# Performance work log

Hardware: AMD Instinct MI355X
Metric: run time of the kernel (lower is better)

The kernel has to match this reference:

```python
import jax, jax.numpy as jnp
import numpy as np

HIDDEN = 2048
GAMMA = 0.96875
SCALE_BASE = 512  # XPOS default from torchscale / Jamie-Stirling/RetNet


def _xpos(x, downscale=False):
    # x: [B, L, d]. Faithful port of XPOS with offset=0.
    B, L, d = x.shape
    half = d // 2
    # per-dim scale vector: (arange(0,d,2) + 0.4d) / (1.4d)
    scale_vec = (jnp.arange(0, d, 2, dtype=jnp.float32) + 0.4 * d) / (1.4 * d)  # [half]
    power = jnp.arange(L, dtype=jnp.float32) / SCALE_BASE                        # [L]
    scale = scale_vec[None, :] ** power[:, None]                                 # [L, half]
    # fixed_pos_embedding over `half` frequency dims
    inv_freq = 1.0 / (10000.0 ** (jnp.arange(half, dtype=jnp.float32) / half))   # [half]
    sinusoid = jnp.arange(L, dtype=jnp.float32)[:, None] * inv_freq[None, :]     # [L, half]
    sin, cos = jnp.sin(sinusoid), jnp.cos(sinusoid)
    if downscale:
        scale = 1.0 / scale
    # duplicate_interleave: [L, half] -> [L, d] with each column repeated twice
    sin_s = jnp.repeat(sin * scale, 2, axis=-1)  # [L, d]
    cos_s = jnp.repeat(cos * scale, 2, axis=-1)  # [L, d]
    # rotate_every_two
    x1 = x[..., 0::2]
    x2 = x[..., 1::2]
    rot = jnp.stack((-x2, x1), axis=-1).reshape(x.shape)
    return x * cos_s[None] + rot * sin_s[None]


def _decay_matrix(L):
    n = jnp.arange(L)[:, None]
    m = jnp.arange(L)[None, :]
    mask = n >= m
    # clamp exponent to avoid overflow where masked (torch sets NaN->0)
    D = jnp.where(mask, GAMMA ** jnp.maximum(n - m, 0).astype(jnp.float32), 0.0)
    return D  # [L, L]


def setup_inputs() -> dict:
    key = jax.random.key(0)
    kx, kq, kk, kv = jax.random.split(key, 4)
    B, S, H = 4, 2048, HIDDEN
    X = jax.random.normal(kx, (B, S, H), dtype=jnp.float32)
    W_Q = jax.random.normal(kq, (H, H), dtype=jnp.float32) / H
    W_K = jax.random.normal(kk, (H, H), dtype=jnp.float32) / H
    W_V = jax.random.normal(kv, (H, H), dtype=jnp.float32) / H
    return {"X": X, "W_Q": W_Q, "W_K": W_K, "W_V": W_V}


def reference(X, W_Q, W_K, W_V):
    B, S, H = X.shape
    Q = _xpos(X @ W_Q)                   # [B, S, H]
    K = _xpos(X @ W_K, downscale=True)   # [B, S, H]
    V = X @ W_V                          # [B, S, H]
    D = _decay_matrix(S)                 # [S, S]
    att = jnp.einsum("bnh,bmh->bnm", Q, K) * D[None]  # [B, S, S]
    return att @ V                       # [B, S, H]
```

## Files before the change

kernel.cpp:

```cpp
#include <hip/hip_runtime.h>
#include <math.h>


typedef __attribute__((ext_vector_type(8))) short short8;
typedef __attribute__((ext_vector_type(4))) float f32x4;
typedef __attribute__((ext_vector_type(4))) unsigned short us4;

#define BM 128
#define ABAND 384

static __device__ __forceinline__ unsigned short f2bf(float f) {
    unsigned int u = __float_as_uint(f);
    u += 0x7FFFu + ((u >> 16) & 1u);
    return (unsigned short)(u >> 16);
}

static __device__ __forceinline__ void gload16(const unsigned short* g, unsigned short* l) {
    __builtin_amdgcn_global_load_lds(
        (const __attribute__((address_space(1))) unsigned int*)g,
        (__attribute__((address_space(3))) unsigned int*)l, 16, 0, 0);
}

template <int STAGE, int BNt, int BKt>
__global__ __launch_bounds__(256)
void gemm_bt(const unsigned short* __restrict__ A,
             const unsigned short* __restrict__ Bt,
             void* __restrict__ Cv,
             unsigned short* __restrict__ Cq,
             unsigned short* __restrict__ Ck,
             unsigned short* __restrict__ Cvt,
             int lda, int ldb, int Kd,
             long long sA, long long sB, long long sC)
{
    constexpr int S = 2048, H = 2048;
    constexpr int NJ = BNt / 32;
    constexpr int KS = BKt / 32;
    constexpr int CR = BKt / 8;
    constexpr int RG = 64 / CR;
    constexpr int GA = 32 / RG;
    constexpr int GB = (BNt / 4) / RG;

    int bx, by, zb;
    if (STAGE == 3) {
        int id = blockIdx.x;
        int swz = (id & 7) * 45 + (id >> 3);
        zb = swz / 90;
        int t = swz - zb * 90;
        if (t < 6) {
            by = (t < 2) ? 0 : 1;
            bx = t - ((by == 0) ? 0 : 2);
        } else {
            by = 2 + (t - 6) / 6;
            bx = ((2 * by - 4) > 0 ? (2 * by - 4) : 0) + (t - 6) % 6;
        }
    } else if (STAGE == 4) {
        int id = blockIdx.x;
        int swz = (id & 7) * 128 + (id >> 3);
        bx = swz >> 6;
        int r = swz & 63;
        zb = r >> 4;
        by = 15 - (r & 15);
    } else {
        bx = blockIdx.x; by = blockIdx.y; zb = 0;
    }
    const int rowBase = by * BM;
    const int colBase = bx * BNt;

    A  += (long long)zb * sA;
    Bt += (long long)zb * sB;

    __shared__ unsigned short As[BM * BKt];
    __shared__ unsigned short Bs[BNt * BKt];

    const int tid  = threadIdx.x;
    const int wave = tid >> 6;
    const int lane = tid & 63;
    const int wm = (wave & 1) * 64;
    const int wn = (wave >> 1) * (BNt / 2);

    f32x4 acc[4][NJ];
#pragma unroll
    for (int i = 0; i < 4; ++i)
#pragma unroll
        for (int j = 0; j < NJ; ++j) acc[i][j] = (f32x4){0.f, 0.f, 0.f, 0.f};

    int kmax = Kd;
    if (STAGE == 4) { int km = rowBase + BM; kmax = km < Kd ? km : Kd; }
    int k0s = 0;
    if (STAGE == 4) {
        int kb0 = 2 * by - 4; k0s = (kb0 > 0 ? kb0 : 0) * 64;
        A -= k0s;
    }

    const int cpos = lane % CR;
    const int rig  = lane / CR;
    const int waveArow = wave * 32;
    const int waveBrow = wave * (BNt / 4);
    unsigned short* lA = As + wave * (32 * BKt);
    unsigned short* lB = Bs + wave * ((BNt / 4) * BKt);

    auto stage_tile = [&](int kb) {
#pragma unroll
        for (int g = 0; g < GA; ++g) {
            int r = waveArow + g * RG + rig;
            gload16(A + (size_t)(rowBase + r) * lda + kb + ((cpos ^ (r & 7)) * 8),
                    lA + g * 512);
        }
#pragma unroll
        for (int g = 0; g < GB; ++g) {
            int r = waveBrow + g * RG + rig;
            gload16(Bt + (size_t)(colBase + r) * ldb + kb + ((cpos ^ (r & 7)) * 8),
                    lB + g * 512);
        }
    };

    stage_tile(k0s);

    const int fr = lane & 15;
    const int qd = lane >> 4;
    const int fsw = fr & 7;

    for (int k0 = k0s; k0 < kmax; k0 += BKt) {
        __syncthreads();
        short8 aF[KS][4], bF[KS][NJ];
#pragma unroll
        for (int kk = 0; kk < KS; ++kk) {
#pragma unroll
            for (int i = 0; i < 4; ++i)
                aF[kk][i] = *(const short8*)&As[(wm + i * 16 + fr) * BKt + (((kk * 4 + qd) ^ fsw) * 8)];
#pragma unroll
            for (int j = 0; j < NJ; ++j)
                bF[kk][j] = *(const short8*)&Bs[(wn + j * 16 + fr) * BKt + (((kk * 4 + qd) ^ fsw) * 8)];
        }
        __syncthreads();
        if (k0 + BKt < kmax) stage_tile(k0 + BKt);
#pragma unroll
        for (int kk = 0; kk < KS; ++kk)
#pragma unroll
            for (int i = 0; i < 4; ++i)
#pragma unroll
                for (int j = 0; j < NJ; ++j)
                    acc[i][j] = __builtin_amdgcn_mfma_f32_16x16x32_bf16(aF[kk][i], bF[kk][j], acc[i][j], 0, 0, 0);
    }

    if (STAGE == 1) {
        const int mode = colBase >> 11;
        if (mode < 2) {
            unsigned short* Co = (mode == 0) ? Cq : Ck;
            const float psgn = (mode == 1) ? -1.953125e-3f : 1.953125e-3f;
#pragma unroll
            for (int j = 0; j < NJ; ++j) {
                int gc = (colBase & 2047) + wn + j * 16 + fr;
                float c0 = (float)(gc & ~1);
                float l2sv = log2f((c0 + 819.2f) * (1.0f / 2867.2f)) * psgn;
                float invf = exp2f(c0 * -0.0064881407f);
                float s1, c1;
                sincosf(invf, &s1, &c1);
#pragma unroll
                for (int i = 0; i < 4; ++i) {
                    int gr0 = rowBase + wm + i * 16 + qd * 4;
                    float fn = (float)(gr0 & (S - 1));
                    float sN, cN;
                    sincosf(fn * invf, &sN, &cN);
#pragma unroll
                    for (int r = 0; r < 4; ++r) {
                        float scale = exp2f(fn * l2sv);
                        float cs = cN * scale, ss = sN * scale;
                        float v = acc[i][j][r];
                        float o = __shfl_xor(v, 1);
                        float res = (gc & 1) ? fmaf(v, cs, o * ss) : fmaf(v, cs, -o * ss);
                        Co[(size_t)(gr0 + r) * H + gc] = f2bf(res);
                        float sn2 = sN * c1 + cN * s1;
                        cN = cN * c1 - sN * s1;
                        sN = sn2;
                        fn += 1.0f;
                    }
                }
            }
        } else {
#pragma unroll
            for (int j = 0; j < NJ; ++j) {
                int gh = (colBase & 2047) + wn + j * 16 + fr;
#pragma unroll
                for (int i = 0; i < 4; ++i) {
                    int gm0 = rowBase + wm + i * 16 + qd * 4;
                    us4 p;
#pragma unroll
                    for (int r = 0; r < 4; ++r) p[r] = f2bf(acc[i][j][r]);
                    *(us4*)&Cvt[(size_t)gh * 8192 + gm0] = p;
                }
            }
        }
    } else if (STAGE == 3) {
        unsigned short* att = (unsigned short*)Cv + (long long)zb * sC;
        const int kb0 = (2 * by - 4) > 0 ? (2 * by - 4) : 0;
        const int mshift = kb0 * 64;
#pragma unroll
        for (int j = 0; j < NJ; ++j) {
            int m = colBase + wn + j * 16 + fr;
#pragma unroll
            for (int i = 0; i < 4; ++i) {
                int n0 = rowBase + wm + i * 16 + qd * 4;
#pragma unroll
                for (int r = 0; r < 4; ++r) {
                    int d = n0 + r - m;
                    float v = (d >= 0) ? acc[i][j][r] * exp2f((float)d * -0.045803598f) : 0.0f;
                    att[(size_t)(n0 + r) * ABAND + (m - mshift)] = f2bf(v);
                }
            }
        }
    } else {
        float* Co = (float*)Cv + (long long)zb * sC;
#pragma unroll
        for (int j = 0; j < NJ; ++j) {
            int gh = colBase + wn + j * 16 + fr;
#pragma unroll
            for (int i = 0; i < 4; ++i) {
                int gn0 = rowBase + wm + i * 16 + qd * 4;
#pragma unroll
                for (int r = 0; r < 4; ++r)
                    Co[(size_t)(gn0 + r) * H + gh] = acc[i][j][r];
            }
        }
    }
}

__global__ __launch_bounds__(256)
void cvt_fused(const float* __restrict__ X, unsigned short* __restrict__ Xb,
               const float* __restrict__ W0, const float* __restrict__ W1,
               const float* __restrict__ W2, unsigned short* __restrict__ Wt) {
    __shared__ float t[64][65];
    if (blockIdx.x < 3072) {
        int id = blockIdx.x;
        int z = id >> 10, rem = id & 1023;
        const float* W = (z == 0) ? W0 : (z == 1) ? W1 : W2;
        unsigned short* Wo = Wt + (size_t)z * 4194304;
        int bx = (rem & 31) * 64, by = (rem >> 5) * 64;
        int tx = threadIdx.x & 63, ty = threadIdx.x >> 6;
#pragma unroll
        for (int r = 0; r < 64; r += 4)
            t[ty + r][tx] = W[(size_t)(by + ty + r) * 2048 + bx + tx];
        __syncthreads();
#pragma unroll
        for (int r = 0; r < 64; r += 4)
            Wo[(size_t)(bx + ty + r) * 2048 + by + tx] = f2bf(t[tx][ty + r]);
    } else {
        int id = blockIdx.x - 3072;
        const float4* X4 = (const float4*)X;
        short8* O8 = (short8*)Xb;
#pragma unroll
        for (int c = 0; c < 4; ++c) {
            size_t u = (size_t)c * (2048 * 256) + (size_t)id * 256 + threadIdx.x;
            float4 a = X4[u * 2];
            float4 b = X4[u * 2 + 1];
            short8 o;
            o[0] = f2bf(a.x); o[1] = f2bf(a.y); o[2] = f2bf(a.z); o[3] = f2bf(a.w);
            o[4] = f2bf(b.x); o[5] = f2bf(b.y); o[6] = f2bf(b.z); o[7] = f2bf(b.w);
            O8[u] = o;
        }
    }
}

extern "C" void kernel_launch(void* const* d_in, const int* in_sizes, int n_in,
                              void* d_out, int out_size, void* d_ws, size_t ws_size,
                              hipStream_t stream) {
    const int S = 2048, H = 2048;
    const long long MH = 16777216;
    const long long HH = 4194304;
    const long long SH = (long long)S * H;
    const long long SB = (long long)S * ABAND;

    const float* X  = (const float*)d_in[0];
    const float* WQ = (const float*)d_in[1];
    const float* WK = (const float*)d_in[2];
    const float* WV = (const float*)d_in[3];
    float* out = (float*)d_out;

    unsigned short* Xb    = (unsigned short*)d_ws;
    unsigned short* WtAll = Xb + MH;
    unsigned short* Qb    = WtAll + 3 * HH;
    unsigned short* Kb    = Qb + MH;
    unsigned short* Vt    = Kb + MH;
    unsigned short* att   = Vt + MH;

    cvt_fused<<<5120, 256, 0, stream>>>(X, Xb, WQ, WK, WV, WtAll);

    gemm_bt<1, 128, 64><<<dim3(48, 64), 256, 0, stream>>>(Xb, WtAll, nullptr, Qb, Kb, Vt,
                                                          H, H, H, 0, 0, 0);
    gemm_bt<3, 64, 128><<<dim3(360, 1, 1), 256, 0, stream>>>(Qb, Kb, att, nullptr, nullptr, nullptr,
                                                             H, H, H, SH, SH, SB);
    gemm_bt<4, 128, 64><<<dim3(1024, 1, 1), 256, 0, stream>>>(att, Vt, out, nullptr, nullptr, nullptr,
                                                              ABAND, 8192, S, SB, 2048, SH);
}
```

Before: 415.1 us.

## Fuse V projection with banded QK^T scores into one heterogeneous launch

Splits the QKV projection so the first launch computes only Q and K (32 column tiles). The V projection tiles then run in the same grid as the banded QK^T score tiles: 360 blocks do attention scores and 1024 blocks do V columns. The goal is to fill the GPU better, since the 360-block score launch alone underuses the CUs, and to hide its tail behind V work. The score GEMM's K-tile also drops from 128 to 64 so both roles can share one shared-memory buffer.

After: 422.0 us (median of 3 runs). Within noise of the previous version (+1.7%).

```diff
diff --git a/kernel.cpp b/kernel.cpp
--- a/kernel.cpp
+++ b/kernel.cpp
@@ -22,15 +22,17 @@
 }
 
 template <int STAGE, int BNt, int BKt>
-__global__ __launch_bounds__(256)
-void gemm_bt(const unsigned short* __restrict__ A,
-             const unsigned short* __restrict__ Bt,
-             void* __restrict__ Cv,
-             unsigned short* __restrict__ Cq,
-             unsigned short* __restrict__ Ck,
-             unsigned short* __restrict__ Cvt,
-             int lda, int ldb, int Kd,
-             long long sA, long long sB, long long sC)
+static __device__ __forceinline__ void gemm_core(
+    const unsigned short* __restrict__ A,
+    const unsigned short* __restrict__ Bt,
+    void* __restrict__ Cv,
+    unsigned short* __restrict__ Cq,
+    unsigned short* __restrict__ Ck,
+    unsigned short* __restrict__ Cvt,
+    int lda, int ldb, int Kd,
+    long long sA, long long sB, long long sC,
+    int bx, int by, int zb,
+    unsigned short* As, unsigned short* Bs)
 {
     constexpr int S = 2048, H = 2048;
     constexpr int NJ = BNt / 32;
@@ -40,37 +42,11 @@
     constexpr int GA = 32 / RG;
     constexpr int GB = (BNt / 4) / RG;
 
-    int bx, by, zb;
-    if (STAGE == 3) {
-        int id = blockIdx.x;
-        int swz = (id & 7) * 45 + (id >> 3);
-        zb = swz / 90;
-        int t = swz - zb * 90;
-        if (t < 6) {
-            by = (t < 2) ? 0 : 1;
-            bx = t - ((by == 0) ? 0 : 2);
-        } else {
-            by = 2 + (t - 6) / 6;
-            bx = ((2 * by - 4) > 0 ? (2 * by - 4) : 0) + (t - 6) % 6;
-        }
-    } else if (STAGE == 4) {
-        int id = blockIdx.x;
-        int swz = (id & 7) * 128 + (id >> 3);
-        bx = swz >> 6;
-        int r = swz & 63;
-        zb = r >> 4;
-        by = 15 - (r & 15);
-    } else {
-        bx = blockIdx.x; by = blockIdx.y; zb = 0;
-    }
     const int rowBase = by * BM;
     const int colBase = bx * BNt;
 
     A  += (long long)zb * sA;
     Bt += (long long)zb * sB;
-
-    __shared__ unsigned short As[BM * BKt];
-    __shared__ unsigned short Bs[BNt * BKt];
 
     const int tid  = threadIdx.x;
     const int wave = tid >> 6;
@@ -225,6 +201,73 @@
     }
 }
 
+template <int STAGE, int BNt, int BKt>
+__global__ __launch_bounds__(256)
+void gemm_bt(const unsigned short* __restrict__ A,
+             const unsigned short* __restrict__ Bt,
+             void* __restrict__ Cv,
+             unsigned short* __restrict__ Cq,
+             unsigned short* __restrict__ Ck,
+             unsigned short* __restrict__ Cvt,
+             int lda, int ldb, int Kd,
+             long long sA, long long sB, long long sC)
+{
+    __shared__ unsigned short As[BM * BKt];
+    __shared__ unsigned short Bs[BNt * BKt];
+    int bx, by, zb;
+    if (STAGE == 4) {
+        int id = blockIdx.x;
+        int swz = (id & 7) * 128 + (id >> 3);
+        bx = swz >> 6;
+        int r = swz & 63;
+        zb = r >> 4;
+        by = 15 - (r & 15);
+    } else {
+        bx = blockIdx.x; by = blockIdx.y; zb = 0;
+    }
+    gemm_core<STAGE, BNt, BKt>(A, Bt, Cv, Cq, Ck, Cvt, lda, ldb, Kd,
+                               sA, sB, sC, bx, by, zb, As, Bs);
+}
+
+__global__ __launch_bounds__(256)
+void fused_vatt(const unsigned short* __restrict__ Xb,
+                const unsigned short* __restrict__ Wt,
+                const unsigned short* __restrict__ Qb,
+                const unsigned short* __restrict__ Kb,
+                unsigned short* __restrict__ att,
+                unsigned short* __restrict__ Vt)
+{
+    constexpr int S = 2048, H = 2048;
+    constexpr long long SH = (long long)S * H;
+    constexpr long long SB = (long long)S * ABAND;
+    __shared__ unsigned short smem[16384];
+    if (blockIdx.x < 360) {
+        int t = blockIdx.x;
+        int swz = (t & 7) * 45 + (t >> 3);
+        int zb = swz / 90;
+        int tt = swz - zb * 90;
+        int bx, by;
+        if (tt < 6) {
+            by = (tt < 2) ? 0 : 1;
+            bx = tt - ((by == 0) ? 0 : 2);
+        } else {
+            by = 2 + (tt - 6) / 6;
+            int kb0 = 2 * by - 4;
+            bx = (kb0 > 0 ? kb0 : 0) + (tt - 6) % 6;
+        }
+        gemm_core<3, 64, 64>(Qb, Kb, att, nullptr, nullptr, nullptr,
+                             H, H, H, SH, SH, SB, bx, by, zb,
+                             smem, smem + 8192);
+    } else {
+        int id = blockIdx.x - 360;
+        int bx = 32 + (id & 15);
+        int by = id >> 4;
+        gemm_core<1, 128, 64>(Xb, Wt, nullptr, nullptr, nullptr, Vt,
+                              H, H, H, 0, 0, 0, bx, by, 0,
+                              smem, smem + 8192);
+    }
+}
+
 __global__ __launch_bounds__(256)
 void cvt_fused(const float* __restrict__ X, unsigned short* __restrict__ Xb,
                const float* __restrict__ W0, const float* __restrict__ W1,
@@ -285,10 +328,10 @@
 
     cvt_fused<<<5120, 256, 0, stream>>>(X, Xb, WQ, WK, WV, WtAll);
 
-    gemm_bt<1, 128, 64><<<dim3(48, 64), 256, 0, stream>>>(Xb, WtAll, nullptr, Qb, Kb, Vt,
+    gemm_bt<1, 128, 64><<<dim3(32, 64), 256, 0, stream>>>(Xb, WtAll, nullptr, Qb, Kb, Vt,
                                                           H, H, H, 0, 0, 0);
-    gemm_bt<3, 64, 128><<<dim3(360, 1, 1), 256, 0, stream>>>(Qb, Kb, att, nullptr, nullptr, nullptr,
-                                                             H, H, H, SH, SH, SB);
-    gemm_bt<4, 128, 64><<<dim3(1024, 1, 1), 256, 0, stream>>>(att, Vt, out, nullptr, nullptr, nullptr,
-                                                              ABAND, 8192, S, SB, 2048, SH);
-}
+    fused_vatt<<<1384, 256, 0, stream>>>(Xb, WtAll, Qb, Kb, att, Vt);
+
+    gemm_bt<4, 128, 64><<<1024, 256, 0, stream>>>(att, Vt, out, nullptr, nullptr, nullptr,
+                                                  ABAND, 8192, S, SB, 2048, SH);
+}
```
